# Performance work log

Measured on AMD Instinct MI355X. Metric: run time of the kernel, lower is better.

## Reference

```python
import jax, jax.numpy as jnp
import numpy as np

B, R, S, D, K = 4096, 49, 50, 512, 100

def setup_inputs() -> dict:
    key = jax.random.key(0)
    ks = jax.random.split(key, 10)
    return {
        "ifeature": jax.random.normal(ks[0], (B, R, D), dtype=jnp.float32),
        "tfeature_h": jax.random.normal(ks[1], (B, S, D), dtype=jnp.float32),
        "w_Vi_0": jax.random.normal(ks[2], (D, K), dtype=jnp.float32) * 0.05,
        "w_Vt_0": jax.random.normal(ks[3], (D, K), dtype=jnp.float32) * 0.05,
        "w_Pi_0": jax.random.normal(ks[4], (2 * K, 1), dtype=jnp.float32) * 0.05,
        "b_Pi_0": jnp.zeros((R,), dtype=jnp.float32),
        "w_Vi_1": jax.random.normal(ks[5], (D, K), dtype=jnp.float32) * 0.05,
        "w_Vt_1": jax.random.normal(ks[6], (D, K), dtype=jnp.float32) * 0.05,
        "w_Pi_1": jax.random.normal(ks[7], (2 * K, 1), dtype=jnp.float32) * 0.05,
        "b_Pi_1": jnp.zeros((S,), dtype=jnp.float32),
    }

def reference(ifeature, tfeature_h, w_Vi_0, w_Vt_0, w_Pi_0, b_Pi_0,
              w_Vi_1, w_Vt_1, w_Pi_1, b_Pi_1):
    # ---- pass 0: attend over image regions, conditioned on mean text feature
    tfeature = jnp.mean(tfeature_h, axis=1)                      # [B, D]
    wVi0 = jnp.einsum('brd,dk->brk', ifeature, w_Vi_0)           # [B, R, K]
    wVt0 = (tfeature @ w_Vt_0)[:, None, :]                       # [B, 1, K] -> broadcast over R
    Hi = jnp.tanh(jnp.concatenate(
        [wVi0, jnp.broadcast_to(wVt0, wVi0.shape)], axis=-1))    # [B, R, 2K]
    scores_i = jnp.squeeze(Hi @ w_Pi_0, axis=-1) + b_Pi_0        # [B, R]
    Pi = jax.nn.softmax(scores_i, axis=-1)                       # [B, R]
    Vi = jnp.einsum('br,brd->bd', Pi, ifeature)                  # [B, D]
    # ---- pass 1: attend over text positions, conditioned on attended image
    wVi1 = (Vi @ w_Vi_1)[:, None, :]                             # [B, 1, K]
    wVt1 = jnp.einsum('bsd,dk->bsk', tfeature_h, w_Vt_1)         # [B, S, K]
    Ht = jnp.tanh(jnp.concatenate(
        [jnp.broadcast_to(wVi1, wVt1.shape), wVt1], axis=-1))    # [B, S, 2K]
    scores_t = jnp.squeeze(Ht @ w_Pi_1, axis=-1) + b_Pi_1        # [B, S]
    Pt = jax.nn.softmax(scores_t, axis=-1)                       # [B, S]
    Vt = jnp.einsum('bs,bsd->bd', Pt, tfeature_h)                # [B, D]
    return Vi + Vt
```

## Files before the change

kernel.cpp:

```cpp
#include <hip/hip_runtime.h>
#include <math.h>

#define NB 4096
#define NR 49
#define NS 50
#define ND 512
#define NK 100
#define NT 7
#define KSTEPS 16
#define CHUNK_KS 8
#define FRAGS (NT * KSTEPS * 64 * 8)

typedef __attribute__((ext_vector_type(8))) short short8;
typedef __attribute__((ext_vector_type(4))) float f32x4;

__device__ __forceinline__ unsigned short f32_bf16(float f) {
    union { float f; unsigned u; } x; x.f = f;
    return (unsigned short)((x.u + 0x7fffu + ((x.u >> 16) & 1u)) >> 16);
}
__device__ __forceinline__ unsigned cvt_pk_bf16(float lo, float hi) {
    unsigned r;
    asm("v_cvt_pk_bf16_f32 %0, %1, %2" : "=v"(r) : "v"(lo), "v"(hi));
    return r;
}
__device__ __forceinline__ float fast_tanh(float x) {
    const float ax = fabsf(x);
    const float e = __expf(2.f * ax);
    const float r = 1.f - 2.f / (e + 1.f);
    return copysignf(r, x);
}

__global__ void preswz_kernel(const float* __restrict__ w0, const float* __restrict__ w1,
                              unsigned short* __restrict__ ws)
{
    const int l  = threadIdx.x;
    const int gk = blockIdx.x & 15;
    const int t  = blockIdx.x >> 4;
    const int m  = blockIdx.y;
    const float* W = m ? w1 : w0;
    const int col = t * 16 + (l & 15);
    const int k0  = gk * 32 + (l >> 4) * 8;
    unsigned short* o = ws + (size_t)m * FRAGS + ((size_t)(t * 16 + gk) * 64 + l) * 8;
#pragma unroll
    for (int j = 0; j < 8; ++j) {
        float v = (col < NK) ? W[(size_t)(k0 + j) * NK + col] : 0.f;
        o[j] = f32_bf16(v);
    }
}

struct SM {
    short buf[NS * 256];
    float scores[64];
    float part2[64];
    float P[64];
};

__global__ __launch_bounds__(512, 4) void coattn_main(
    const float* __restrict__ ifeat, const float* __restrict__ tfeat,
    const float* __restrict__ wPi0, const float* __restrict__ bPi0,
    const float* __restrict__ wPi1, const float* __restrict__ bPi1,
    const unsigned short* __restrict__ wsW, float* __restrict__ out)
{
    __shared__ SM sm;
    const int pass = blockIdx.x & 1;
    const int b    = blockIdx.x >> 1;
    const int tid  = threadIdx.x;

    const float* feat = pass ? (tfeat + (size_t)b * NS * ND) : (ifeat + (size_t)b * NR * ND);
    const int nrows  = pass ? NS : NR;
    const int nclamp = nrows - 1;
    const unsigned short* wsR = wsW + (size_t)pass * FRAGS;
    const float* wPiRow = pass ? (wPi1 + NK) : wPi0;
    const float* bvec   = pass ? bPi1 : bPi0;

    const int lane = tid & 63, wid = tid >> 6;
    const int m = wid & 3, nh = wid >> 2;
    const int t0 = nh * 4, tcnt = nh ? 3 : 4;
    const int colg = lane & 15, g = lane >> 4;
    const int arow0 = m * 16 + colg;
    const int arow = (arow0 < nclamp) ? arow0 : nclamp;
    const int rswz = arow & 7;

    const unsigned short* wbase[4];
#pragma unroll
    for (int q = 0; q < 4; ++q)
        wbase[q] = wsR + (size_t)(t0 + q) * (KSTEPS * 512) + lane * 8;

    const f32x4 zero4 = {0.f, 0.f, 0.f, 0.f};
    f32x4 acc[4] = {zero4, zero4, zero4, zero4};

    const int nitems = nrows * 32;

    for (int chunk = 0; chunk < 2; ++chunk) {
        __syncthreads();
        for (int it = tid; it < nitems; it += 512) {
            const int r = it >> 5, c = it & 31;
            const float* p = feat + (r << 9) + (chunk << 8) + (c << 3);
            const float4 a  = *reinterpret_cast<const float4*>(p);
            const float4 b4 = *reinterpret_cast<const float4*>(p + 4);
            uint4 v;
            v.x = cvt_pk_bf16(a.x, a.y);   v.y = cvt_pk_bf16(a.z, a.w);
            v.z = cvt_pk_bf16(b4.x, b4.y); v.w = cvt_pk_bf16(b4.z, b4.w);
            *reinterpret_cast<uint4*>(&sm.buf[(r << 8) + ((c ^ (r & 7)) << 3)]) = v;
        }
        __syncthreads();

        const int gk0 = chunk * CHUNK_KS;
        short8 wf[2][4];
#pragma unroll
        for (int s = 0; s < 2; ++s)
#pragma unroll
            for (int q = 0; q < 4; ++q)
                if (q < tcnt) wf[s][q] = *reinterpret_cast<const short8*>(wbase[q] + (gk0 + s) * 512);

#pragma unroll
        for (int ks = 0; ks < CHUNK_KS; ++ks) {
            const short8 a = *reinterpret_cast<const short8*>(
                &sm.buf[(arow << 8) + ((((ks << 2) + g) ^ rswz) << 3)]);
            short8 cur[4];
#pragma unroll
            for (int q = 0; q < 4; ++q) cur[q] = wf[ks & 1][q];
            if (ks + 2 < CHUNK_KS) {
#pragma unroll
                for (int q = 0; q < 4; ++q)
                    if (q < tcnt) wf[ks & 1][q] = *reinterpret_cast<const short8*>(wbase[q] + (gk0 + ks + 2) * 512);
            }
#pragma unroll
            for (int q = 0; q < 4; ++q)
                if (q < tcnt) acc[q] = __builtin_amdgcn_mfma_f32_16x16x32_bf16(a, cur[q], acc[q], 0, 0, 0);
        }
    }

    {
        float s[4] = {0.f, 0.f, 0.f, 0.f};
#pragma unroll
        for (int q = 0; q < 4; ++q)
            if (q < tcnt) {
                const int col = (t0 + q) * 16 + colg;
                const float w = (col < NK) ? wPiRow[col] : 0.f;
#pragma unroll
                for (int i = 0; i < 4; ++i) s[i] += fast_tanh(acc[q][i]) * w;
            }
#pragma unroll
        for (int off = 1; off < 16; off <<= 1) {
#pragma unroll
            for (int i = 0; i < 4; ++i) s[i] += __shfl_xor(s[i], off);
        }
        if (colg == 0) {
            float* o = nh ? sm.part2 : sm.scores;
            const int rbase = m * 16 + g * 4;
#pragma unroll
            for (int i = 0; i < 4; ++i) {
                const int r = rbase + i;
                if (r < nrows) o[r] = s[i] + (nh ? 0.f : bvec[r]);
            }
        }
    }
    __syncthreads();

    if (tid < 64) {
        const float v = (tid < nrows) ? sm.scores[tid] + sm.part2[tid] : -3.0e38f;
        float mx = v;
#pragma unroll
        for (int off = 32; off; off >>= 1) mx = fmaxf(mx, __shfl_xor(mx, off));
        const float e = (tid < nrows) ? __expf(v - mx) : 0.f;
        float su = e;
#pragma unroll
        for (int off = 32; off; off >>= 1) su += __shfl_xor(su, off);
        sm.P[tid] = e / su;
    }
    __syncthreads();

    {
        float v = 0.f;
        const float* fp = feat + tid;
        for (int r = 0; r < nrows; ++r) v += sm.P[r] * fp[r << 9];
        atomicAdd(&out[(size_t)b * ND + tid], v);
    }
}

extern "C" void kernel_launch(void* const* d_in, const int* in_sizes, int n_in,
                              void* d_out, int out_size, void* d_ws, size_t ws_size,
                              hipStream_t stream) {
    const float* ifeat = (const float*)d_in[0];
    const float* tfeat = (const float*)d_in[1];
    const float* wVi0  = (const float*)d_in[2];
    const float* wPi0  = (const float*)d_in[4];
    const float* bPi0  = (const float*)d_in[5];
    const float* wVt1  = (const float*)d_in[7];
    const float* wPi1  = (const float*)d_in[8];
    const float* bPi1  = (const float*)d_in[9];
    float* outp = (float*)d_out;
    unsigned short* wsW = (unsigned short*)d_ws;

    hipMemsetAsync(outp, 0, (size_t)NB * ND * sizeof(float), stream);
    hipLaunchKernelGGL(preswz_kernel, dim3(NT * KSTEPS, 2), dim3(64), 0, stream,
                       wVi0, wVt1, wsW);
    hipLaunchKernelGGL(coattn_main, dim3(2 * NB), dim3(512), 0, stream,
                       ifeat, tfeat, wPi0, bPi0, wPi1, bPi1, wsW, outp);
}
```

Measured before the change: 315.9 us.

## Pad weight tiles to eight, drop register prefetch, raise occupancy bound

Pads the pre-swizzled weight fragments from 7 to 8 column tiles so every wave handles exactly 4 tiles with no tcnt branch. It removes the double-buffered register prefetch of weight fragments and loads them directly before each MFMA. It raises the launch-bounds minimum blocks to 8 to cut register pressure and increase occupancy. The trade-off is exposed global/L2 load latency inside the MFMA loop plus wasted MFMA work on the all-zero padded tile, in exchange for more resident waves to hide that latency.

```diff
diff --git a/kernel.cpp b/kernel.cpp
--- a/kernel.cpp
+++ b/kernel.cpp
@@ -6,10 +6,10 @@
 #define NS 50
 #define ND 512
 #define NK 100
-#define NT 7
+#define NTT 8
 #define KSTEPS 16
 #define CHUNK_KS 8
-#define FRAGS (NT * KSTEPS * 64 * 8)
+#define FRAGS (NTT * KSTEPS * 64 * 8)
 
 typedef __attribute__((ext_vector_type(8))) short short8;
 typedef __attribute__((ext_vector_type(4))) float f32x4;
@@ -55,7 +55,7 @@
     float P[64];
 };
 
-__global__ __launch_bounds__(512, 4) void coattn_main(
+__global__ __launch_bounds__(512, 8) void coattn_main(
     const float* __restrict__ ifeat, const float* __restrict__ tfeat,
     const float* __restrict__ wPi0, const float* __restrict__ bPi0,
     const float* __restrict__ wPi1, const float* __restrict__ bPi1,
@@ -75,16 +75,13 @@
 
     const int lane = tid & 63, wid = tid >> 6;
     const int m = wid & 3, nh = wid >> 2;
-    const int t0 = nh * 4, tcnt = nh ? 3 : 4;
+    const int t0 = nh * 4;
     const int colg = lane & 15, g = lane >> 4;
     const int arow0 = m * 16 + colg;
     const int arow = (arow0 < nclamp) ? arow0 : nclamp;
     const int rswz = arow & 7;
 
-    const unsigned short* wbase[4];
-#pragma unroll
-    for (int q = 0; q < 4; ++q)
-        wbase[q] = wsR + (size_t)(t0 + q) * (KSTEPS * 512) + lane * 8;
+    const unsigned short* wlane = wsR + (size_t)t0 * (KSTEPS * 512) + lane * 8;
 
     const f32x4 zero4 = {0.f, 0.f, 0.f, 0.f};
     f32x4 acc[4] = {zero4, zero4, zero4, zero4};
@@ -106,41 +103,28 @@
         __syncthreads();
 
         const int gk0 = chunk * CHUNK_KS;
-        short8 wf[2][4];
-#pragma unroll
-        for (int s = 0; s < 2; ++s)
-#pragma unroll
-            for (int q = 0; q < 4; ++q)
-                if (q < tcnt) wf[s][q] = *reinterpret_cast<const short8*>(wbase[q] + (gk0 + s) * 512);
-
 #pragma unroll
         for (int ks = 0; ks < CHUNK_KS; ++ks) {
             const short8 a = *reinterpret_cast<const short8*>(
                 &sm.buf[(arow << 8) + ((((ks << 2) + g) ^ rswz) << 3)]);
-            short8 cur[4];
+            const unsigned short* wk = wlane + (size_t)(gk0 + ks) * 512;
 #pragma unroll
-            for (int q = 0; q < 4; ++q) cur[q] = wf[ks & 1][q];
-            if (ks + 2 < CHUNK_KS) {
-#pragma unroll
-                for (int q = 0; q < 4; ++q)
-                    if (q < tcnt) wf[ks & 1][q] = *reinterpret_cast<const short8*>(wbase[q] + (gk0 + ks + 2) * 512);
+            for (int q = 0; q < 4; ++q) {
+                const short8 w = *reinterpret_cast<const short8*>(wk + (size_t)q * (KSTEPS * 512));
+                acc[q] = __builtin_amdgcn_mfma_f32_16x16x32_bf16(a, w, acc[q], 0, 0, 0);
             }
-#pragma unroll
-            for (int q = 0; q < 4; ++q)
-                if (q < tcnt) acc[q] = __builtin_amdgcn_mfma_f32_16x16x32_bf16(a, cur[q], acc[q], 0, 0, 0);
         }
     }
 
     {
         float s[4] = {0.f, 0.f, 0.f, 0.f};
 #pragma unroll
-        for (int q = 0; q < 4; ++q)
-            if (q < tcnt) {
-                const int col = (t0 + q) * 16 + colg;
-                const float w = (col < NK) ? wPiRow[col] : 0.f;
+        for (int q = 0; q < 4; ++q) {
+            const int col = (t0 + q) * 16 + colg;
+            const float w = (col < NK) ? wPiRow[col] : 0.f;
 #pragma unroll
-                for (int i = 0; i < 4; ++i) s[i] += fast_tanh(acc[q][i]) * w;
-            }
+            for (int i = 0; i < 4; ++i) s[i] += fast_tanh(acc[q][i]) * w;
+        }
 #pragma unroll
         for (int off = 1; off < 16; off <<= 1) {
 #pragma unroll
@@ -194,7 +178,7 @@
     unsigned short* wsW = (unsigned short*)d_ws;
 
     hipMemsetAsync(outp, 0, (size_t)NB * ND * sizeof(float), stream);
-    hipLaunchKernelGGL(preswz_kernel, dim3(NT * KSTEPS, 2), dim3(64), 0, stream,
+    hipLaunchKernelGGL(preswz_kernel, dim3(NTT * KSTEPS, 2), dim3(64), 0, stream,
                        wVi0, wVt1, wsW);
     hipLaunchKernelGGL(coattn_main, dim3(2 * NB), dim3(512), 0, stream,
                        ifeat, tfeat, wPi0, bPi0, wPi1, bPi1, wsW, outp);
```

Result: slower. 338.9 us (+7.3%).

## Assign one output column tile per wave and iterate all row tiles

Applied to the files above, without the earlier changes.

Reorganizes the MFMA work split so each of 7 waves owns one 16-column weight tile and loops over all 4 row tiles, loading each weight fragment once from global memory and reusing it across row tiles. LDS activation reads go up fourfold per wave, while global weight loads and the register-held weight prefetch buffers are removed. The eighth wave is idle during the matmul, and the score reduction now sums seven per-wave partials in shared memory.

```diff
diff --git a/kernel.cpp b/kernel.cpp
--- a/kernel.cpp
+++ b/kernel.cpp
@@ -50,8 +50,7 @@
 
 struct SM {
     short buf[NS * 256];
-    float scores[64];
-    float part2[64];
+    float part[NT][64];
     float P[64];
 };
 
@@ -74,20 +73,18 @@
     const float* bvec   = pass ? bPi1 : bPi0;
 
     const int lane = tid & 63, wid = tid >> 6;
-    const int m = wid & 3, nh = wid >> 2;
-    const int t0 = nh * 4, tcnt = nh ? 3 : 4;
     const int colg = lane & 15, g = lane >> 4;
-    const int arow0 = m * 16 + colg;
-    const int arow = (arow0 < nclamp) ? arow0 : nclamp;
-    const int rswz = arow & 7;
-
-    const unsigned short* wbase[4];
-#pragma unroll
-    for (int q = 0; q < 4; ++q)
-        wbase[q] = wsR + (size_t)(t0 + q) * (KSTEPS * 512) + lane * 8;
 
     const f32x4 zero4 = {0.f, 0.f, 0.f, 0.f};
     f32x4 acc[4] = {zero4, zero4, zero4, zero4};
+
+    int arow_[4], rswz_[4];
+#pragma unroll
+    for (int rt = 0; rt < 4; ++rt) {
+        const int r0 = rt * 16 + colg;
+        arow_[rt] = (r0 < nclamp) ? r0 : nclamp;
+        rswz_[rt] = arow_[rt] & 7;
+    }
 
     const int nitems = nrows * 32;
 
@@ -105,61 +102,54 @@
         }
         __syncthreads();
 
-        const int gk0 = chunk * CHUNK_KS;
-        short8 wf[2][4];
+        if (wid < NT) {
+            const unsigned short* wl = wsR
+                + ((size_t)(wid * KSTEPS + chunk * CHUNK_KS) * 64 + lane) * 8;
 #pragma unroll
-        for (int s = 0; s < 2; ++s)
+            for (int ks = 0; ks < CHUNK_KS; ++ks) {
+                const short8 w = *reinterpret_cast<const short8*>(wl + ks * 512);
+                const int q0 = (ks << 2) + g;
 #pragma unroll
-            for (int q = 0; q < 4; ++q)
-                if (q < tcnt) wf[s][q] = *reinterpret_cast<const short8*>(wbase[q] + (gk0 + s) * 512);
-
-#pragma unroll
-        for (int ks = 0; ks < CHUNK_KS; ++ks) {
-            const short8 a = *reinterpret_cast<const short8*>(
-                &sm.buf[(arow << 8) + ((((ks << 2) + g) ^ rswz) << 3)]);
-            short8 cur[4];
-#pragma unroll
-            for (int q = 0; q < 4; ++q) cur[q] = wf[ks & 1][q];
-            if (ks + 2 < CHUNK_KS) {
-#pragma unroll
-                for (int q = 0; q < 4; ++q)
-                    if (q < tcnt) wf[ks & 1][q] = *reinterpret_cast<const short8*>(wbase[q] + (gk0 + ks + 2) * 512);
+                for (int rt = 0; rt < 4; ++rt) {
+                    const short8 a = *reinterpret_cast<const short8*>(
+                        &sm.buf[(arow_[rt] << 8) + ((q0 ^ rswz_[rt]) << 3)]);
+                    acc[rt] = __builtin_amdgcn_mfma_f32_16x16x32_bf16(a, w, acc[rt], 0, 0, 0);
+                }
             }
-#pragma unroll
-            for (int q = 0; q < 4; ++q)
-                if (q < tcnt) acc[q] = __builtin_amdgcn_mfma_f32_16x16x32_bf16(a, cur[q], acc[q], 0, 0, 0);
         }
     }
 
-    {
-        float s[4] = {0.f, 0.f, 0.f, 0.f};
+    if (wid < NT) {
+        const int col = wid * 16 + colg;
+        const float w = (col < NK) ? wPiRow[col] : 0.f;
+        float sp[4][4];
 #pragma unroll
-        for (int q = 0; q < 4; ++q)
-            if (q < tcnt) {
-                const int col = (t0 + q) * 16 + colg;
-                const float w = (col < NK) ? wPiRow[col] : 0.f;
+        for (int rt = 0; rt < 4; ++rt)
 #pragma unroll
-                for (int i = 0; i < 4; ++i) s[i] += fast_tanh(acc[q][i]) * w;
-            }
+            for (int i = 0; i < 4; ++i)
+                sp[rt][i] = fast_tanh(acc[rt][i]) * w;
 #pragma unroll
-        for (int off = 1; off < 16; off <<= 1) {
+        for (int off = 1; off < 16; off <<= 1)
 #pragma unroll
-            for (int i = 0; i < 4; ++i) s[i] += __shfl_xor(s[i], off);
-        }
+            for (int rt = 0; rt < 4; ++rt)
+#pragma unroll
+                for (int i = 0; i < 4; ++i)
+                    sp[rt][i] += __shfl_xor(sp[rt][i], off);
         if (colg == 0) {
-            float* o = nh ? sm.part2 : sm.scores;
-            const int rbase = m * 16 + g * 4;
 #pragma unroll
-            for (int i = 0; i < 4; ++i) {
-                const int r = rbase + i;
-                if (r < nrows) o[r] = s[i] + (nh ? 0.f : bvec[r]);
-            }
+            for (int rt = 0; rt < 4; ++rt)
+#pragma unroll
+                for (int i = 0; i < 4; ++i)
+                    sm.part[wid][rt * 16 + g * 4 + i] = sp[rt][i];
         }
     }
     __syncthreads();
 
     if (tid < 64) {
-        const float v = (tid < nrows) ? sm.scores[tid] + sm.part2[tid] : -3.0e38f;
+        float v = (tid < nrows) ? bvec[tid] : 0.f;
+#pragma unroll
+        for (int w = 0; w < NT; ++w) v += sm.part[w][tid];
+        v = (tid < nrows) ? v : -3.0e38f;
         float mx = v;
 #pragma unroll
         for (int off = 32; off; off >>= 1) mx = fmaxf(mx, __shfl_xor(mx, off));
```

Measured after the change: 306.4 us. 3.0% less time.
